# Performance work log

Hardware: AMD Instinct MI355X
Metric: run time of the kernel (lower is better)

Reference implementation:

```python
import jax, jax.numpy as jnp
import numpy as np

B, N, C = 8, 4096, 512

def setup_inputs() -> dict:
    key = jax.random.key(0)
    ks = jax.random.split(key, 6)
    s = 1.0 / np.sqrt(C)
    return {
        "x": jax.random.normal(ks[0], (B, N, C), jnp.float32),
        "Wq": jax.random.normal(ks[1], (C, C), jnp.float32) * s,
        "Wk": jax.random.normal(ks[2], (C, C), jnp.float32) * s,
        "Wv": jax.random.normal(ks[3], (C, C), jnp.float32) * s,
        "W1": jax.random.normal(ks[4], (C, C), jnp.float32) * s,
        "W2": jax.random.normal(ks[5], (C, C), jnp.float32) * s,
    }

def reference(x, Wq, Wk, Wv, W1, W2):
    # torch nn.Linear: y = x @ W.T (bias=False)
    q = x @ Wq.T                      # [B,N,C]
    k = x @ Wk.T
    v = x @ Wv.T
    dim = q.shape[-1]
    q = jax.nn.softmax(q, axis=-1) * (dim ** -0.5)   # softmax over channels
    k = jax.nn.softmax(k, axis=-2)                   # softmax over sequence
    context = jnp.einsum('bnd,bne->bde', k, v)       # [B,C,C]
    attn = jnp.einsum('bnd,bde->bne', q, context)    # [B,N,C]
    x = attn + x
    return (x @ W1.T) @ W2.T + x
```

## Files before the change

### kernel.cpp

```cpp
#include <hip/hip_runtime.h>

typedef unsigned int uint;
typedef __bf16 bf16_t;
typedef bf16_t bf16x8 __attribute__((ext_vector_type(8)));
typedef float floatx4 __attribute__((ext_vector_type(4)));

struct __align__(8) us4 { unsigned short x, y, z, w; };

__device__ __forceinline__ unsigned short f2b(float f) {
    unsigned u = __float_as_uint(f);
    u = u + 0x7FFFu + ((u >> 16) & 1u);
    return (unsigned short)(u >> 16);
}
__device__ __forceinline__ float b2f(unsigned short h) {
    return __uint_as_float(((unsigned)h) << 16);
}

__device__ __forceinline__ void g2l16(const void* g, void* l) {
    __builtin_amdgcn_global_load_lds((__attribute__((address_space(1))) void*)g,
                                     (__attribute__((address_space(3))) void*)l,
                                     16, 0, 0);
}

template <int MODE, int NT, bool BMS>
__global__ __launch_bounds__(256, 4) void gemm64(
    const unsigned short* __restrict__ A, const unsigned short* __restrict__ B,
    void* __restrict__ O, const unsigned short* __restrict__ R,
    unsigned short* __restrict__ O2, unsigned short* __restrict__ O3,
    float* __restrict__ Sq, float* __restrict__ Sk,
    const float* __restrict__ Sn,
    int K, int lda, int ldb, int ldo, long long sB, float scale)
{
    __shared__ __attribute__((aligned(16))) unsigned short As[128 * 64];
    __shared__ __attribute__((aligned(16))) unsigned short Bs[128 * 64];

    const uint id = blockIdx.x;
    const uint xcd = id & 7;
    const uint g = id >> 3;
    const uint nt = g % NT;
    const uint mg = g / NT;
    const uint ms = mg * 8 + xcd;

    int bb, arow0;
    if constexpr (BMS) { bb = ms & 7; arow0 = bb * 4096 + (int)(ms >> 3) * 128; }
    else               { bb = 0;      arow0 = (int)ms * 128; }
    const int n0 = (int)nt * 128;

    const unsigned short* Bb = B + (long long)bb * sB;
    const int tid = threadIdx.x;
    const int l = tid & 63;
    const int w = tid >> 6;
    const int wm = (w >> 1) * 64;
    const int wn = (w & 1) * 64;

    const int srow = tid >> 3;
    const int scol = (tid & 7) * 8;
    const unsigned short* ga = A + (long long)(arow0 + srow) * lda + scol;
    const unsigned short* gb = Bb + (long long)(n0 + srow) * ldb + scol;
    unsigned short* la = As + tid * 8;
    unsigned short* lb = Bs + tid * 8;

    const int fr = l & 15;
    const int kq = (l >> 4) * 8;

    floatx4 acc[4][4] = {};

    for (int kt = 0; kt < K; kt += 64) {
        __syncthreads();
#pragma unroll
        for (int c = 0; c < 4; ++c) {
            g2l16(ga + (long long)(c * 32) * lda, la + c * 2048);
            g2l16(gb + (long long)(c * 32) * ldb, lb + c * 2048);
        }
        ga += 64; gb += 64;
        __syncthreads();

#pragma unroll
        for (int h = 0; h < 2; ++h) {
            bf16x8 af[4], bfr[4];
#pragma unroll
            for (int i = 0; i < 4; ++i) {
                af[i]  = *(const bf16x8*)(As + (wm + i * 16 + fr) * 64 + kq + 32 * h);
                bfr[i] = *(const bf16x8*)(Bs + (wn + i * 16 + fr) * 64 + kq + 32 * h);
            }
#pragma unroll
            for (int i = 0; i < 4; ++i)
#pragma unroll
                for (int j = 0; j < 4; ++j)
                    acc[i][j] = __builtin_amdgcn_mfma_f32_16x16x32_bf16(
                        af[i], bfr[j], acc[i][j], 0, 0, 0);
        }
    }

    const int col = l & 15;
    const int rbase = (l >> 4) * 4;

    if constexpr (MODE == 4) {
        if (n0 < 512) {
            unsigned short* Oq = (unsigned short*)O;
            float rs[4][4];
#pragma unroll
            for (int i = 0; i < 4; ++i)
#pragma unroll
                for (int r = 0; r < 4; ++r) rs[i][r] = 0.f;
#pragma unroll
            for (int i = 0; i < 4; ++i)
#pragma unroll
                for (int j = 0; j < 4; ++j) {
                    int gn = n0 + wn + j * 16 + col;
                    int gmb = arow0 + wm + i * 16 + rbase;
#pragma unroll
                    for (int r = 0; r < 4; ++r) {
                        float e = __expf(acc[i][j][r]);
                        rs[i][r] += e;
                        Oq[(long long)(gmb + r) * 512 + gn] = f2b(e);
                    }
                }
#pragma unroll
            for (int i = 0; i < 4; ++i)
#pragma unroll
                for (int r = 0; r < 4; ++r) {
                    float v = rs[i][r];
                    v += __shfl_xor(v, 1);
                    v += __shfl_xor(v, 2);
                    v += __shfl_xor(v, 4);
                    v += __shfl_xor(v, 8);
                    if ((l & 15) == 0)
                        atomicAdd(&Sq[arow0 + wm + i * 16 + rbase + r], v);
                }
        } else if (n0 < 1024) {
            const int b = arow0 >> 12;
            const int mq0 = arow0 & 4095;
            float cs[4] = {0.f, 0.f, 0.f, 0.f};
#pragma unroll
            for (int i = 0; i < 4; ++i)
#pragma unroll
                for (int j = 0; j < 4; ++j) {
                    int d = n0 + wn + j * 16 + col - 512;
                    int mq = mq0 + wm + i * 16 + rbase;
                    float e0 = __expf(acc[i][j][0]);
                    float e1 = __expf(acc[i][j][1]);
                    float e2 = __expf(acc[i][j][2]);
                    float e3 = __expf(acc[i][j][3]);
                    cs[j] += e0 + e1 + e2 + e3;
                    us4 pk = { f2b(e0), f2b(e1), f2b(e2), f2b(e3) };
                    *(us4*)(O2 + ((long long)b * 512 + d) * 4096 + mq) = pk;
                }
#pragma unroll
            for (int j = 0; j < 4; ++j) {
                float v = cs[j];
                v += __shfl_xor(v, 16);
                v += __shfl_xor(v, 32);
                if (l < 16)
                    atomicAdd(&Sk[b * 512 + n0 + wn + j * 16 + col - 512], v);
            }
        } else {
            const int b = arow0 >> 12;
            const int mq0 = arow0 & 4095;
#pragma unroll
            for (int i = 0; i < 4; ++i)
#pragma unroll
                for (int j = 0; j < 4; ++j) {
                    int e = n0 + wn + j * 16 + col - 1024;
                    int mq = mq0 + wm + i * 16 + rbase;
                    us4 pk = { f2b(acc[i][j][0]), f2b(acc[i][j][1]),
                               f2b(acc[i][j][2]), f2b(acc[i][j][3]) };
                    *(us4*)(O3 + ((long long)b * 512 + e) * 4096 + mq) = pk;
                }
        }
    } else if constexpr (MODE == 5) {
#pragma unroll
        for (int i = 0; i < 4; ++i) {
            int gmb = arow0 + wm + i * 16 + rbase;
            float invs[4];
#pragma unroll
            for (int r = 0; r < 4; ++r) invs[r] = scale / Sn[gmb + r];
#pragma unroll
            for (int j = 0; j < 4; ++j) {
                int gn = n0 + wn + j * 16 + col;
#pragma unroll
                for (int r = 0; r < 4; ++r) {
                    long long idx = (long long)(gmb + r) * ldo + gn;
                    ((unsigned short*)O)[idx] =
                        f2b(acc[i][j][r] * invs[r] + b2f(R[idx]));
                }
            }
        }
    } else {
#pragma unroll
        for (int i = 0; i < 4; ++i)
#pragma unroll
            for (int j = 0; j < 4; ++j) {
                int gn = n0 + wn + j * 16 + col;
                int gmb = arow0 + wm + i * 16 + rbase;
#pragma unroll
                for (int r = 0; r < 4; ++r) {
                    long long idx = (long long)(gmb + r) * ldo + gn;
                    float v = acc[i][j][r];
                    if constexpr (MODE == 0) {
                        ((unsigned short*)O)[idx] = f2b(v);
                    } else {
                        ((float*)O)[idx] = v + b2f(R[idx]);
                    }
                }
            }
    }
}

__global__ __launch_bounds__(256, 4) void ctx_gemm_sk(
    const unsigned short* __restrict__ V, const unsigned short* __restrict__ Kt,
    float* __restrict__ P)
{
    __shared__ __attribute__((aligned(16))) unsigned short As[128 * 64];
    __shared__ __attribute__((aligned(16))) unsigned short Bs[128 * 64];

    const uint id = blockIdx.x;
    const uint xcd = id & 7;
    const uint g = id >> 3;
    const uint sub = g & 15;
    const int z = (int)(g >> 4) * 8 + (int)xcd;
    const int b = z >> 2;
    const int s = z & 3;
    const int m0 = (int)(sub >> 2) * 128;
    const int n0 = (int)(sub & 3) * 128;

    const unsigned short* Ab = V  + (long long)b * 512 * 4096 + s * 1024;
    const unsigned short* Bb = Kt + (long long)b * 512 * 4096 + s * 1024;

    const int tid = threadIdx.x;
    const int l = tid & 63;
    const int w = tid >> 6;
    const int wm = (w >> 1) * 64;
    const int wn = (w & 1) * 64;

    const int srow = tid >> 3;
    const int scol = (tid & 7) * 8;
    const unsigned short* ga = Ab + (long long)(m0 + srow) * 4096 + scol;
    const unsigned short* gb = Bb + (long long)(n0 + srow) * 4096 + scol;
    unsigned short* la = As + tid * 8;
    unsigned short* lb = Bs + tid * 8;

    const int fr = l & 15;
    const int kq = (l >> 4) * 8;

    floatx4 acc[4][4] = {};

    for (int kt = 0; kt < 1024; kt += 64) {
        __syncthreads();
#pragma unroll
        for (int c = 0; c < 4; ++c) {
            g2l16(ga + (long long)(c * 32) * 4096, la + c * 2048);
            g2l16(gb + (long long)(c * 32) * 4096, lb + c * 2048);
        }
        ga += 64; gb += 64;
        __syncthreads();

#pragma unroll
        for (int h = 0; h < 2; ++h) {
            bf16x8 af[4], bfr[4];
#pragma unroll
            for (int i = 0; i < 4; ++i) {
                af[i]  = *(const bf16x8*)(As + (wm + i * 16 + fr) * 64 + kq + 32 * h);
                bfr[i] = *(const bf16x8*)(Bs + (wn + i * 16 + fr) * 64 + kq + 32 * h);
            }
#pragma unroll
            for (int i = 0; i < 4; ++i)
#pragma unroll
                for (int j = 0; j < 4; ++j)
                    acc[i][j] = __builtin_amdgcn_mfma_f32_16x16x32_bf16(
                        af[i], bfr[j], acc[i][j], 0, 0, 0);
        }
    }

    const int col = l & 15;
    const int rbase = (l >> 4) * 4;
    float* Pb = P + ((long long)z * 16 + (sub >> 2) * 4 + (sub & 3)) * 16384;
#pragma unroll
    for (int i = 0; i < 4; ++i)
#pragma unroll
        for (int j = 0; j < 4; ++j)
#pragma unroll
            for (int r = 0; r < 4; ++r)
                Pb[(wm + i * 16 + rbase + r) * 128 + wn + j * 16 + col] =
                    acc[i][j][r];
}

__global__ __launch_bounds__(256) void ctx_reduce(const float* __restrict__ P,
                                                  const float* __restrict__ Sk,
                                                  unsigned short* __restrict__ Ct)
{
    long long f = (long long)blockIdx.x * 256 + threadIdx.x;
    long long base = f * 4;
    int tile = (int)(base >> 14);
    int lo = (int)(base & 16383);
    int b = tile >> 4;
    int mt = (tile >> 2) & 3;
    int nt = tile & 3;
    float4 s = {0.f, 0.f, 0.f, 0.f};
#pragma unroll
    for (int sp = 0; sp < 4; ++sp) {
        float4 v = *(const float4*)(P + ((long long)(b * 4 + sp) * 16 + mt * 4 + nt) * 16384 + lo);
        s.x += v.x; s.y += v.y; s.z += v.z; s.w += v.w;
    }
    int le = lo >> 7;
    int ld = lo & 127;
    float4 sk = *(const float4*)(Sk + b * 512 + nt * 128 + ld);
    us4 o = { f2b(s.x / sk.x), f2b(s.y / sk.y), f2b(s.z / sk.z), f2b(s.w / sk.w) };
    *(us4*)(Ct + (long long)b * 262144 + (mt * 128 + le) * 512 + nt * 128 + ld) = o;
}

__global__ __launch_bounds__(256) void f32_to_bf16_k(const float* __restrict__ in,
                                                     unsigned short* __restrict__ out)
{
    long long i = ((long long)blockIdx.x * 256 + threadIdx.x) * 4;
    float4 v = *(const float4*)(in + i);
    us4 o = { f2b(v.x), f2b(v.y), f2b(v.z), f2b(v.w) };
    *(us4*)(out + i) = o;
}

struct WPtrs { const float* in[5]; unsigned short* out[5]; };
__global__ __launch_bounds__(256) void conv_weights(WPtrs p)
{
    int which = blockIdx.y;
    long long i = ((long long)blockIdx.x * 256 + threadIdx.x) * 4;
    float4 v = *(const float4*)(p.in[which] + i);
    us4 o = { f2b(v.x), f2b(v.y), f2b(v.z), f2b(v.w) };
    *(us4*)(p.out[which] + i) = o;
}

__global__ __launch_bounds__(256) void zero_f32(float* __restrict__ p)
{
    long long i = ((long long)blockIdx.x * 256 + threadIdx.x) * 4;
    *(float4*)(p + i) = make_float4(0.f, 0.f, 0.f, 0.f);
}

extern "C" void kernel_launch(void* const* d_in, const int* in_sizes, int n_in,
                              void* d_out, int out_size, void* d_ws, size_t ws_size,
                              hipStream_t stream)
{
    (void)in_sizes; (void)n_in; (void)out_size; (void)ws_size;
    const float* x  = (const float*)d_in[0];
    const float* Wq = (const float*)d_in[1];
    const float* Wk = (const float*)d_in[2];
    const float* Wv = (const float*)d_in[3];
    const float* W1 = (const float*)d_in[4];
    const float* W2 = (const float*)d_in[5];
    float* out = (float*)d_out;

    const int Bn = 8, N = 4096, C = 512;
    const long long M  = (long long)Bn * N;
    const long long XE = M * C;

    char* ws = (char*)d_ws;
    size_t off = 0;
    auto carve = [&](size_t bytes) -> void* {
        void* p = ws + off;
        off += (bytes + 255) & ~(size_t)255;
        return p;
    };

    unsigned short* xb   = (unsigned short*)carve(XE * 2);
    unsigned short* wcat = (unsigned short*)carve((size_t)3 * C * C * 2);
    unsigned short* w1b  = (unsigned short*)carve((size_t)C * C * 2);
    unsigned short* w2b  = (unsigned short*)carve((size_t)C * C * 2);
    unsigned short* q    = (unsigned short*)carve(XE * 2);
    unsigned short* kT   = (unsigned short*)carve(XE * 2);
    unsigned short* vT   = (unsigned short*)carve(XE * 2);
    unsigned short* ctxT = (unsigned short*)carve((size_t)Bn * C * C * 2);
    float* Ssum = (float*)carve((size_t)(M + Bn * C) * 4);
    float* Sq = Ssum;
    float* Sk = Ssum + M;
    unsigned short* xr = kT;
    unsigned short* h  = vT;
    float* P = (float*)d_out;

    zero_f32<<<dim3(36), 256, 0, stream>>>(Ssum);

    f32_to_bf16_k<<<dim3((unsigned)(XE / 1024)), dim3(256), 0, stream>>>(x, xb);
    WPtrs wp = { { Wq, Wk, Wv, W1, W2 },
                 { wcat, wcat + C * C, wcat + 2 * C * C, w1b, w2b } };
    conv_weights<<<dim3((C * C) / 1024, 5), dim3(256), 0, stream>>>(wp);

    gemm64<4, 12, false><<<dim3(3072), 256, 0, stream>>>(
        xb, wcat, q, nullptr, kT, vT, Sq, Sk, nullptr, C, C, C, C, 0, 0.f);

    ctx_gemm_sk<<<dim3(512), 256, 0, stream>>>(vT, kT, P);
    ctx_reduce<<<dim3(2048), 256, 0, stream>>>(P, Sk, ctxT);

    gemm64<5, 4, true><<<dim3(1024), 256, 0, stream>>>(
        q, ctxT, xr, xb, nullptr, nullptr, nullptr, nullptr, Sq,
        C, C, C, C, (long long)C * C, 0.044194173824159216f);

    gemm64<0, 4, false><<<dim3(1024), 256, 0, stream>>>(
        xr, w1b, h, nullptr, nullptr, nullptr, nullptr, nullptr, nullptr,
        C, C, C, C, 0, 0.f);

    gemm64<3, 4, false><<<dim3(1024), 256, 0, stream>>>(
        h, w2b, out, xr, nullptr, nullptr, nullptr, nullptr, nullptr,
        C, C, C, C, 0, 0.f);
}
```

Baseline: 312.0 us.

## Replace 128x128 GEMM with 256x256-tile, 4-stage pipelined swizzled-LDS GEMM

Rewrites the shared GEMM kernel to use 256x256 output tiles with 512 threads, a BK=32 four-buffer LDS ring filled by async global-to-LDS loads, and XOR-swizzled LDS addressing. Each wave now computes a 128x64 sub-tile with 32 MFMA accumulators. The aim is more data reuse per loaded byte, fewer LDS bank conflicts, and overlap of the next tile's loads with the current tile's MFMAs. The trade-offs are higher register and LDS pressure and fewer blocks: 256 blocks for the 512-wide GEMMs on a 256-CU part, which risks poor tail occupancy.

```diff
diff --git a/kernel.cpp b/kernel.cpp
--- a/kernel.cpp
+++ b/kernel.cpp
@@ -22,102 +22,123 @@
                                      16, 0, 0);
 }
 
-template <int MODE, int NT, bool BMS>
-__global__ __launch_bounds__(256, 4) void gemm64(
+template <int MODE, int NTN, bool BMS>
+__global__ __launch_bounds__(512, 2) void gemm256(
     const unsigned short* __restrict__ A, const unsigned short* __restrict__ B,
     void* __restrict__ O, const unsigned short* __restrict__ R,
     unsigned short* __restrict__ O2, unsigned short* __restrict__ O3,
     float* __restrict__ Sq, float* __restrict__ Sk,
     const float* __restrict__ Sn,
-    int K, int lda, int ldb, int ldo, long long sB, float scale)
-{
-    __shared__ __attribute__((aligned(16))) unsigned short As[128 * 64];
-    __shared__ __attribute__((aligned(16))) unsigned short Bs[128 * 64];
+    int K, long long sB, float scale)
+{
+    __shared__ __attribute__((aligned(16))) unsigned short Ls[4][16384];
 
     const uint id = blockIdx.x;
     const uint xcd = id & 7;
     const uint g = id >> 3;
-    const uint nt = g % NT;
-    const uint mg = g / NT;
+    const uint nt = g % NTN;
+    const uint mg = g / NTN;
     const uint ms = mg * 8 + xcd;
 
     int bb, arow0;
-    if constexpr (BMS) { bb = ms & 7; arow0 = bb * 4096 + (int)(ms >> 3) * 128; }
-    else               { bb = 0;      arow0 = (int)ms * 128; }
-    const int n0 = (int)nt * 128;
+    if constexpr (BMS) { bb = (int)(ms & 7); arow0 = bb * 4096 + (int)(ms >> 3) * 256; }
+    else               { bb = 0;             arow0 = (int)ms * 256; }
+    const int n0 = (int)nt * 256;
 
     const unsigned short* Bb = B + (long long)bb * sB;
     const int tid = threadIdx.x;
     const int l = tid & 63;
     const int w = tid >> 6;
-    const int wm = (w >> 1) * 64;
-    const int wn = (w & 1) * 64;
-
-    const int srow = tid >> 3;
-    const int scol = (tid & 7) * 8;
-    const unsigned short* ga = A + (long long)(arow0 + srow) * lda + scol;
-    const unsigned short* gb = Bb + (long long)(n0 + srow) * ldb + scol;
-    unsigned short* la = As + tid * 8;
-    unsigned short* lb = Bs + tid * 8;
+
+    const int r0 = tid >> 3;
+    const int lc = (tid & 7) ^ (r0 & 7);
+    const unsigned short* gsrc = (lc < 4)
+        ? A  + (long long)(arow0 + r0) * 512 + lc * 8
+        : Bb + (long long)(n0   + r0) * 512 + (lc - 4) * 8;
+
+#define STAGE(bufi, tt) {                                                   \
+        const unsigned short* s_ = gsrc + (tt) * 32;                        \
+        unsigned short* d_ = &Ls[bufi][0] + tid * 8;                        \
+        g2l16(s_,              d_);                                         \
+        g2l16(s_ + 64  * 512,  d_ + 4096);                                  \
+        g2l16(s_ + 128 * 512,  d_ + 8192);                                  \
+        g2l16(s_ + 192 * 512,  d_ + 12288);                                 \
+    }
 
     const int fr = l & 15;
     const int kq = (l >> 4) * 8;
-
-    floatx4 acc[4][4] = {};
-
-    for (int kt = 0; kt < K; kt += 64) {
-        __syncthreads();
-#pragma unroll
-        for (int c = 0; c < 4; ++c) {
-            g2l16(ga + (long long)(c * 32) * lda, la + c * 2048);
-            g2l16(gb + (long long)(c * 32) * ldb, lb + c * 2048);
-        }
-        ga += 64; gb += 64;
-        __syncthreads();
-
-#pragma unroll
-        for (int h = 0; h < 2; ++h) {
-            bf16x8 af[4], bfr[4];
-#pragma unroll
-            for (int i = 0; i < 4; ++i) {
-                af[i]  = *(const bf16x8*)(As + (wm + i * 16 + fr) * 64 + kq + 32 * h);
-                bfr[i] = *(const bf16x8*)(Bs + (wn + i * 16 + fr) * 64 + kq + 32 * h);
-            }
-#pragma unroll
-            for (int i = 0; i < 4; ++i)
-#pragma unroll
-                for (int j = 0; j < 4; ++j)
-                    acc[i][j] = __builtin_amdgcn_mfma_f32_16x16x32_bf16(
-                        af[i], bfr[j], acc[i][j], 0, 0, 0);
+    const int axA = (kq * 2) ^ ((fr & 7) << 4);
+    const int axB = axA ^ 64;
+    const int wr = w >> 2;
+    const int wc = w & 3;
+
+    floatx4 acc[8][4] = {};
+    const int NTk = K >> 5;
+
+    STAGE(0, 0); STAGE(1, 1); STAGE(2, 2);
+    asm volatile("s_waitcnt vmcnt(8)" ::: "memory");
+    __builtin_amdgcn_s_barrier();
+
+    for (int t = 0; t < NTk; ++t) {
+        if (t + 3 < NTk) STAGE((t + 3) & 3, t + 3);
+
+        const char* Lb = (const char*)&Ls[t & 3][0];
+        const char* pa = Lb + (wr * 128 + fr) * 128 + axA;
+        const char* pb = Lb + (wc * 64  + fr) * 128 + axB;
+
+        bf16x8 af[8], bv[4];
+#pragma unroll
+        for (int i = 0; i < 8; ++i) af[i] = *(const bf16x8*)(pa + i * 2048);
+#pragma unroll
+        for (int j = 0; j < 4; ++j) bv[j] = *(const bf16x8*)(pb + j * 2048);
+
+        __builtin_amdgcn_s_setprio(1);
+#pragma unroll
+        for (int i = 0; i < 8; ++i)
+#pragma unroll
+            for (int j = 0; j < 4; ++j)
+                acc[i][j] = __builtin_amdgcn_mfma_f32_16x16x32_bf16(
+                    af[i], bv[j], acc[i][j], 0, 0, 0);
+        __builtin_amdgcn_s_setprio(0);
+
+        if (t < NTk - 1) {
+            if (t + 3 < NTk)      asm volatile("s_waitcnt vmcnt(8)" ::: "memory");
+            else if (t + 2 < NTk) asm volatile("s_waitcnt vmcnt(4)" ::: "memory");
+            else                  asm volatile("s_waitcnt vmcnt(0)" ::: "memory");
+            __builtin_amdgcn_s_barrier();
         }
     }
+#undef STAGE
 
     const int col = l & 15;
     const int rbase = (l >> 4) * 4;
+    const int gm0 = arow0 + wr * 128 + rbase;
+    const int gn0 = n0 + wc * 64 + col;
 
     if constexpr (MODE == 4) {
         if (n0 < 512) {
             unsigned short* Oq = (unsigned short*)O;
-            float rs[4][4];
-#pragma unroll
-            for (int i = 0; i < 4; ++i)
+            float rs[8][4];
+#pragma unroll
+            for (int i = 0; i < 8; ++i)
 #pragma unroll
                 for (int r = 0; r < 4; ++r) rs[i][r] = 0.f;
 #pragma unroll
-            for (int i = 0; i < 4; ++i)
+            for (int i = 0; i < 8; ++i) {
+                int gm = gm0 + i * 16;
 #pragma unroll
                 for (int j = 0; j < 4; ++j) {
-                    int gn = n0 + wn + j * 16 + col;
-                    int gmb = arow0 + wm + i * 16 + rbase;
+                    int gn = gn0 + j * 16;
 #pragma unroll
                     for (int r = 0; r < 4; ++r) {
                         float e = __expf(acc[i][j][r]);
                         rs[i][r] += e;
-                        Oq[(long long)(gmb + r) * 512 + gn] = f2b(e);
+                        Oq[(long long)(gm + r) * 512 + gn] = f2b(e);
                     }
                 }
-#pragma unroll
-            for (int i = 0; i < 4; ++i)
+            }
+#pragma unroll
+            for (int i = 0; i < 8; ++i)
 #pragma unroll
                 for (int r = 0; r < 4; ++r) {
                     float v = rs[i][r];
@@ -126,18 +147,18 @@
                     v += __shfl_xor(v, 4);
                     v += __shfl_xor(v, 8);
                     if ((l & 15) == 0)
-                        atomicAdd(&Sq[arow0 + wm + i * 16 + rbase + r], v);
+                        atomicAdd(&Sq[gm0 + i * 16 + r], v);
                 }
         } else if (n0 < 1024) {
             const int b = arow0 >> 12;
-            const int mq0 = arow0 & 4095;
+            const int mq0 = (arow0 & 4095) + wr * 128 + rbase;
             float cs[4] = {0.f, 0.f, 0.f, 0.f};
 #pragma unroll
-            for (int i = 0; i < 4; ++i)
+            for (int i = 0; i < 8; ++i) {
+                int mq = mq0 + i * 16;
 #pragma unroll
                 for (int j = 0; j < 4; ++j) {
-                    int d = n0 + wn + j * 16 + col - 512;
-                    int mq = mq0 + wm + i * 16 + rbase;
+                    int d = gn0 + j * 16 - 512;
                     float e0 = __expf(acc[i][j][0]);
                     float e1 = __expf(acc[i][j][1]);
                     float e2 = __expf(acc[i][j][2]);
@@ -146,41 +167,43 @@
                     us4 pk = { f2b(e0), f2b(e1), f2b(e2), f2b(e3) };
                     *(us4*)(O2 + ((long long)b * 512 + d) * 4096 + mq) = pk;
                 }
+            }
 #pragma unroll
             for (int j = 0; j < 4; ++j) {
                 float v = cs[j];
                 v += __shfl_xor(v, 16);
                 v += __shfl_xor(v, 32);
                 if (l < 16)
-                    atomicAdd(&Sk[b * 512 + n0 + wn + j * 16 + col - 512], v);
+                    atomicAdd(&Sk[b * 512 + gn0 + j * 16 - 512], v);
             }
         } else {
             const int b = arow0 >> 12;
-            const int mq0 = arow0 & 4095;
-#pragma unroll
-            for (int i = 0; i < 4; ++i)
+            const int mq0 = (arow0 & 4095) + wr * 128 + rbase;
+#pragma unroll
+            for (int i = 0; i < 8; ++i) {
+                int mq = mq0 + i * 16;
 #pragma unroll
                 for (int j = 0; j < 4; ++j) {
-                    int e = n0 + wn + j * 16 + col - 1024;
-                    int mq = mq0 + wm + i * 16 + rbase;
+                    int e_ = gn0 + j * 16 - 1024;
                     us4 pk = { f2b(acc[i][j][0]), f2b(acc[i][j][1]),
                                f2b(acc[i][j][2]), f2b(acc[i][j][3]) };
-                    *(us4*)(O3 + ((long long)b * 512 + e) * 4096 + mq) = pk;
-                }
+                    *(us4*)(O3 + ((long long)b * 512 + e_) * 4096 + mq) = pk;
+                }
+            }
         }
     } else if constexpr (MODE == 5) {
 #pragma unroll
-        for (int i = 0; i < 4; ++i) {
-            int gmb = arow0 + wm + i * 16 + rbase;
+        for (int i = 0; i < 8; ++i) {
+            int gm = gm0 + i * 16;
             float invs[4];
 #pragma unroll
-            for (int r = 0; r < 4; ++r) invs[r] = scale / Sn[gmb + r];
+            for (int r = 0; r < 4; ++r) invs[r] = scale / Sn[gm + r];
 #pragma unroll
             for (int j = 0; j < 4; ++j) {
-                int gn = n0 + wn + j * 16 + col;
+                int gn = gn0 + j * 16;
 #pragma unroll
                 for (int r = 0; r < 4; ++r) {
-                    long long idx = (long long)(gmb + r) * ldo + gn;
+                    long long idx = (long long)(gm + r) * 512 + gn;
                     ((unsigned short*)O)[idx] =
                         f2b(acc[i][j][r] * invs[r] + b2f(R[idx]));
                 }
@@ -188,14 +211,14 @@
         }
     } else {
 #pragma unroll
-        for (int i = 0; i < 4; ++i)
+        for (int i = 0; i < 8; ++i) {
+            int gm = gm0 + i * 16;
 #pragma unroll
             for (int j = 0; j < 4; ++j) {
-                int gn = n0 + wn + j * 16 + col;
-                int gmb = arow0 + wm + i * 16 + rbase;
+                int gn = gn0 + j * 16;
 #pragma unroll
                 for (int r = 0; r < 4; ++r) {
-                    long long idx = (long long)(gmb + r) * ldo + gn;
+                    long long idx = (long long)(gm + r) * 512 + gn;
                     float v = acc[i][j][r];
                     if constexpr (MODE == 0) {
                         ((unsigned short*)O)[idx] = f2b(v);
@@ -204,6 +227,7 @@
                     }
                 }
             }
+        }
     }
 }
 
@@ -381,21 +405,21 @@
                  { wcat, wcat + C * C, wcat + 2 * C * C, w1b, w2b } };
     conv_weights<<<dim3((C * C) / 1024, 5), dim3(256), 0, stream>>>(wp);
 
-    gemm64<4, 12, false><<<dim3(3072), 256, 0, stream>>>(
-        xb, wcat, q, nullptr, kT, vT, Sq, Sk, nullptr, C, C, C, C, 0, 0.f);
+    gemm256<4, 6, false><<<dim3(768), 512, 0, stream>>>(
+        xb, wcat, q, nullptr, kT, vT, Sq, Sk, nullptr, C, 0, 0.f);
 
     ctx_gemm_sk<<<dim3(512), 256, 0, stream>>>(vT, kT, P);
     ctx_reduce<<<dim3(2048), 256, 0, stream>>>(P, Sk, ctxT);
 
-    gemm64<5, 4, true><<<dim3(1024), 256, 0, stream>>>(
+    gemm256<5, 2, true><<<dim3(256), 512, 0, stream>>>(
         q, ctxT, xr, xb, nullptr, nullptr, nullptr, nullptr, Sq,
-        C, C, C, C, (long long)C * C, 0.044194173824159216f);
-
-    gemm64<0, 4, false><<<dim3(1024), 256, 0, stream>>>(
+        C, (long long)C * C, 0.044194173824159216f);
+
+    gemm256<0, 2, false><<<dim3(256), 512, 0, stream>>>(
         xr, w1b, h, nullptr, nullptr, nullptr, nullptr, nullptr, nullptr,
-        C, C, C, C, 0, 0.f);
-
-    gemm64<3, 4, false><<<dim3(1024), 256, 0, stream>>>(
+        C, 0, 0.f);
+
+    gemm256<3, 2, false><<<dim3(256), 512, 0, stream>>>(
         h, w2b, out, xr, nullptr, nullptr, nullptr, nullptr, nullptr,
-        C, C, C, C, 0, 0.f);
-}
+        C, 0, 0.f);
+}
```

Result: faster. 302.3 us (-3.1%).
